# Optimization experiments

Hardware: AMD Instinct MI355X
Metric: run time of the kernel (lower is better)

Reference implementation:

```python
import jax, jax.numpy as jnp
import numpy as np

A, T, N_GRID, RBF, F = 128, 2048, 65536, 16, 128
L_DIMS = (1, 3, 5)  # irreps 0e, 1e, 2e


def setup_inputs() -> dict:
    key = jax.random.key(0)
    ks = jax.random.split(key, 16)
    nrm = lambda k, s, sc=1.0: jax.random.normal(k, s, dtype=jnp.float32) * sc
    w_sc = 1.0 / np.sqrt(F).astype(np.float32)
    return {
        "feat0": nrm(ks[0], (A, F, 1)),
        "feat1": nrm(ks[1], (A, F, 3)),
        "feat2": nrm(ks[2], (A, F, 5)),
        "sph0": nrm(ks[3], (A, T, 1)),
        "sph1": nrm(ks[4], (A, T, 3)),
        "sph2": nrm(ks[5], (A, T, 5)),
        "radial_basis_vals": jax.random.uniform(ks[6], (A, T, RBF), dtype=jnp.float32),
        "mlp_w1": nrm(ks[7], (3, F, F), w_sc),
        "mlp_b1": jnp.zeros((3, F), jnp.float32),
        "mlp_w2": nrm(ks[8], (3, F, F), w_sc),
        "mlp_b2": jnp.zeros((3, F), jnp.float32),
        "mlp_w3": nrm(ks[9], (3, F, RBF * F), w_sc),
        "mlp_b3": jnp.zeros((3, RBF * F), jnp.float32),
        "truncated_idx": jax.random.randint(ks[10], (T,), 0, N_GRID, dtype=jnp.int32),
        "N": N_GRID,
    }


def reference(feat0, feat1, feat2, sph0, sph1, sph2, radial_basis_vals,
              mlp_w1, mlp_b1, mlp_w2, mlp_b2, mlp_w3, mlp_b3,
              truncated_idx, N):
    f_dim = feat0.shape[1]
    rbf = radial_basis_vals.shape[-1]
    inv_features = feat0[..., 0]  # (A, F) scalar (0e) channel
    inv_rbf = jnp.asarray(1.0 / np.sqrt(rbf), dtype=feat0.dtype)
    feats = (feat0, feat1, feat2)
    sphs = (sph0, sph1, sph2)
    spatial_features = jnp.zeros((N, f_dim), dtype=feat0.dtype)
    for i in range(3):  # fixed small loop over irrep chunks
        h = jax.nn.silu(inv_features @ mlp_w1[i] + mlp_b1[i])
        h = jax.nn.silu(h @ mlp_w2[i] + mlp_b2[i])
        rbf_to_f = (h @ mlp_w3[i] + mlp_b3[i]).reshape(-1, rbf, f_dim) * inv_rbf  # (A, RBF, F)
        # reduce over atoms n, sph index d, radial index r -> (T, F)
        sparse = jnp.einsum('ntd,nfd,ntr,nrf->tf', sphs[i], feats[i],
                            radial_basis_vals, rbf_to_f)
        spatial_features = spatial_features.at[truncated_idx].add(sparse)
    return spatial_features
```

## Files before the change

### kernel.cpp

```cpp
#include <hip/hip_runtime.h>
#include <hip/hip_bf16.h>
#include <cstdint>
#include <cstddef>

#define A_DIM 128
#define T_DIM 2048
#define F_DIM 128
#define RBF_DIM 16
#define KDD 2048
#define VT_LD 18432
#define NKG 32
#define BT 64

typedef __attribute__((ext_vector_type(8))) short short8;
typedef __attribute__((ext_vector_type(4))) float f32x4;
typedef __attribute__((ext_vector_type(4))) unsigned int u32x4;

__device__ __forceinline__ float silu_f(float x) {
    return x / (1.0f + __expf(-x));
}

__device__ __forceinline__ unsigned short f2bf(float x) {
    union { float f; unsigned u; } v; v.f = x;
    unsigned r = v.u + 0x7FFFu + ((v.u >> 16) & 1u);
    return (unsigned short)(r >> 16);
}

__device__ __forceinline__ void gl_lds16(const void* g, void* l) {
    __builtin_amdgcn_global_load_lds(
        (const __attribute__((address_space(1))) void*)g,
        (__attribute__((address_space(3))) void*)l, 16, 0, 0);
}

__global__ void zero_kernel(float4* __restrict__ p, int n4) {
    const int stride = gridDim.x * blockDim.x;
    const float4 z = {0.f, 0.f, 0.f, 0.f};
    for (int i = blockIdx.x * blockDim.x + threadIdx.x; i < n4; i += stride)
        p[i] = z;
}

__global__ void mlp_fused_kernel(const float* __restrict__ feat0,
                                 const float* __restrict__ w1, const float* __restrict__ b1,
                                 const float* __restrict__ w2, const float* __restrict__ b2,
                                 const float* __restrict__ w3, const float* __restrict__ b3,
                                 float* __restrict__ rbfws) {
    __shared__ float inv_s[4 * F_DIM];
    __shared__ float h_s[4 * F_DIM];
    __shared__ float h2_s[4 * F_DIM];
    const int i  = blockIdx.y;
    const int a0 = blockIdx.x * 4;
    const int tid = threadIdx.x;
    const int f  = tid & 127;
    const int la = tid >> 7;

    inv_s[tid] = feat0[(a0 + la) * F_DIM + f];
    __syncthreads();

    const float* w1i = w1 + (size_t)i * F_DIM * F_DIM;
    float x = b1[i * F_DIM + f];
    #pragma unroll 8
    for (int k = 0; k < F_DIM; ++k)
        x = fmaf(inv_s[la * F_DIM + k], w1i[k * F_DIM + f], x);
    h_s[tid] = silu_f(x);
    __syncthreads();

    const float* w2i = w2 + (size_t)i * F_DIM * F_DIM;
    float y = b2[i * F_DIM + f];
    #pragma unroll 8
    for (int k = 0; k < F_DIM; ++k)
        y = fmaf(h_s[la * F_DIM + k], w2i[k * F_DIM + f], y);
    h2_s[tid] = silu_f(y);
    __syncthreads();

    const int c = tid * 4;
    const float* w3i = w3 + (size_t)i * F_DIM * 2048;
    float val[4][4];
    #pragma unroll
    for (int a = 0; a < 4; ++a) {
        #pragma unroll
        for (int cc = 0; cc < 4; ++cc)
            val[a][cc] = b3[i * 2048 + c + cc];
    }
    for (int k = 0; k < F_DIM; ++k) {
        const float4 w = *reinterpret_cast<const float4*>(&w3i[(size_t)k * 2048 + c]);
        #pragma unroll
        for (int a = 0; a < 4; ++a) {
            const float h = h2_s[a * F_DIM + k];
            val[a][0] = fmaf(h, w.x, val[a][0]);
            val[a][1] = fmaf(h, w.y, val[a][1]);
            val[a][2] = fmaf(h, w.z, val[a][2]);
            val[a][3] = fmaf(h, w.w, val[a][3]);
        }
    }
    const float inv_rbf = 0.25f;
    #pragma unroll
    for (int a = 0; a < 4; ++a) {
        float4 o;
        o.x = val[a][0] * inv_rbf;
        o.y = val[a][1] * inv_rbf;
        o.z = val[a][2] * inv_rbf;
        o.w = val[a][3] * inv_rbf;
        *reinterpret_cast<float4*>(&rbfws[((size_t)i * A_DIM + a0 + a) * 2048 + c]) = o;
    }
}

__global__ void build_vt_kernel(const float* __restrict__ feat0,
                                const float* __restrict__ feat1,
                                const float* __restrict__ feat2,
                                const float* __restrict__ rbfws,
                                unsigned short* __restrict__ Vt) {
    const int n  = blockIdx.x;
    const int dd = blockIdx.y;
    const int f  = threadIdx.x;

    int i, d;
    float fv;
    if (dd == 0)      { i = 0; d = 0;      fv = feat0[n * F_DIM + f]; }
    else if (dd < 4)  { i = 1; d = dd - 1; fv = feat1[(n * F_DIM + f) * 3 + d]; }
    else              { i = 2; d = dd - 4; fv = feat2[(n * F_DIM + f) * 5 + d]; }

    const float* rb = rbfws + ((size_t)(i * A_DIM + n) * RBF_DIM) * F_DIM + f;
    unsigned short* vp = Vt + (size_t)f * VT_LD + (size_t)dd * KDD + n * 16;
    #pragma unroll
    for (int r = 0; r < RBF_DIM; ++r)
        vp[r] = f2bf(fv * rb[(size_t)r * F_DIM]);
}

template<int MODE>
__global__ void __launch_bounds__(256) gemm_kernel(
        const float* __restrict__ sph0, const float* __restrict__ sph1,
        const float* __restrict__ sph2, const float* __restrict__ radial,
        const unsigned short* __restrict__ Vt,
        float* __restrict__ outbuf,
        float* __restrict__ dout, int out_n4) {
    __shared__ unsigned short b_s[F_DIM * 64];
    __shared__ float sph_s[4 * BT];

    const int tid  = threadIdx.x;
    const int lane = tid & 63;
    const int w    = tid >> 6;
    const int wr   = w >> 1;
    const int wc   = w & 1;
    const int t0   = blockIdx.x * BT + wr * 32;
    const int n0   = blockIdx.y * 4;
    const int kq   = lane >> 4;
    const int lf   = lane & 15;

    if (MODE == 0) {
        const int bid = blockIdx.y * gridDim.x + blockIdx.x;
        const float4 z = {0.f, 0.f, 0.f, 0.f};
        float4* zp = (float4*)dout;
        #pragma unroll
        for (int q = 0; q < 8; ++q) {
            const int idx = bid * 2048 + q * 256 + tid;
            if (idx < out_n4) zp[idx] = z;
        }
    }

    f32x4 rad[2][2][2];
    #pragma unroll
    for (int m = 0; m < 2; ++m) {
        const int t = t0 + 16 * m + lf;
        #pragma unroll
        for (int ks = 0; ks < 2; ++ks) {
            const int n = n0 + 2 * ks + (kq >> 1);
            const float* rp = radial + ((size_t)n * T_DIM + t) * 16 + (kq & 1) * 8;
            rad[m][ks][0] = *reinterpret_cast<const f32x4*>(rp);
            rad[m][ks][1] = *reinterpret_cast<const f32x4*>(rp + 4);
        }
    }

    const int fs_row = tid >> 3;
    const int cs     = (tid & 7) ^ ((tid >> 3) & 7);
    const unsigned short* gsrc0 = Vt + (size_t)fs_row * VT_LD + n0 * 16 + cs * 8;
    const int nn_s = tid >> 6;
    const int tt_s = tid & 63;
    const size_t sph_tbase = (size_t)(n0 + nn_s) * T_DIM + blockIdx.x * BT + tt_s;

    f32x4 acc[2][4];
    #pragma unroll
    for (int m = 0; m < 2; ++m)
        #pragma unroll
        for (int nf = 0; nf < 4; ++nf)
            acc[m][nf] = (f32x4){0.f, 0.f, 0.f, 0.f};

    #pragma unroll 1
    for (int dd = 0; dd < 9; ++dd) {
        const float* sp; int smul, soff;
        if (dd == 0)     { sp = sph0; smul = 1; soff = 0; }
        else if (dd < 4) { sp = sph1; smul = 3; soff = dd - 1; }
        else             { sp = sph2; smul = 5; soff = dd - 4; }

        __syncthreads();

        const size_t koff = (size_t)dd * KDD;
        #pragma unroll
        for (int q = 0; q < 4; ++q) {
            const unsigned short* gp = gsrc0 + koff + (size_t)(q * 32) * VT_LD;
            void* lp = (void*)((char*)b_s + q * 4096 + w * 1024);
            gl_lds16(gp, lp);
        }
        sph_s[tid] = sp[sph_tbase * smul + soff];

        __syncthreads();

        short8 bfr[2][4];
        #pragma unroll
        for (int ks = 0; ks < 2; ++ks) {
            #pragma unroll
            for (int nf = 0; nf < 4; ++nf) {
                const int f = wc * 64 + 16 * nf + lf;
                const int byte = f * 128 + (((ks * 4 + kq) ^ (lf & 7)) * 16);
                bfr[ks][nf] = *reinterpret_cast<const short8*>((const char*)b_s + byte);
            }
        }

        #pragma unroll
        for (int m = 0; m < 2; ++m) {
            #pragma unroll
            for (int ks = 0; ks < 2; ++ks) {
                const float s = sph_s[(2 * ks + (kq >> 1)) * BT + wr * 32 + 16 * m + lf];
                unsigned int d0, d1, d2, d3;
                asm("v_cvt_pk_bf16_f32 %0, %1, %2" : "=v"(d0)
                    : "v"(s * rad[m][ks][0][0]), "v"(s * rad[m][ks][0][1]));
                asm("v_cvt_pk_bf16_f32 %0, %1, %2" : "=v"(d1)
                    : "v"(s * rad[m][ks][0][2]), "v"(s * rad[m][ks][0][3]));
                asm("v_cvt_pk_bf16_f32 %0, %1, %2" : "=v"(d2)
                    : "v"(s * rad[m][ks][1][0]), "v"(s * rad[m][ks][1][1]));
                asm("v_cvt_pk_bf16_f32 %0, %1, %2" : "=v"(d3)
                    : "v"(s * rad[m][ks][1][2]), "v"(s * rad[m][ks][1][3]));
                union { u32x4 u; short8 s8; } au;
                au.u = (u32x4){d0, d1, d2, d3};
                #pragma unroll
                for (int nf = 0; nf < 4; ++nf)
                    acc[m][nf] = __builtin_amdgcn_mfma_f32_16x16x32_bf16(
                        au.s8, bfr[ks][nf], acc[m][nf], 0, 0, 0);
            }
        }
    }

    float* pb = (MODE == 0)
        ? outbuf + (size_t)blockIdx.y * (T_DIM * F_DIM)
        : outbuf;
    #pragma unroll
    for (int m = 0; m < 2; ++m) {
        #pragma unroll
        for (int nf = 0; nf < 4; ++nf) {
            const int f = wc * 64 + 16 * nf + lf;
            #pragma unroll
            for (int reg = 0; reg < 4; ++reg) {
                const int t = t0 + 16 * m + 4 * kq + reg;
                if (MODE == 0)
                    pb[(size_t)t * F_DIM + f] = acc[m][nf][reg];
                else
                    atomicAdd(&pb[(size_t)t * F_DIM + f], acc[m][nf][reg]);
            }
        }
    }
}

__global__ void scatter_sum_kernel(const float* __restrict__ partial,
                                   const int* __restrict__ tidx,
                                   float* __restrict__ out) {
    const int tid = threadIdx.x;
    const int t = blockIdx.x * 2 + (tid >> 7);
    const int f = tid & 127;
    const int g = tidx[t];
    const float* p = partial + (size_t)t * F_DIM + f;
    float s = 0.0f;
    #pragma unroll
    for (int kg = 0; kg < NKG; ++kg)
        s += p[(size_t)kg * (T_DIM * F_DIM)];
    atomicAdd(&out[(size_t)g * F_DIM + f], s);
}

__global__ void scatter_kernel(const float* __restrict__ sparse,
                               const int* __restrict__ tidx,
                               float* __restrict__ out) {
    const int tid = threadIdx.x;
    const int t = blockIdx.x * 2 + (tid >> 7);
    const int f = tid & 127;
    const int g = tidx[t];
    atomicAdd(&out[(size_t)g * F_DIM + f], sparse[(size_t)t * F_DIM + f]);
}

extern "C" void kernel_launch(void* const* d_in, const int* in_sizes, int n_in,
                              void* d_out, int out_size, void* d_ws, size_t ws_size,
                              hipStream_t stream) {
    const float* feat0  = (const float*)d_in[0];
    const float* feat1  = (const float*)d_in[1];
    const float* feat2  = (const float*)d_in[2];
    const float* sph0   = (const float*)d_in[3];
    const float* sph1   = (const float*)d_in[4];
    const float* sph2   = (const float*)d_in[5];
    const float* radial = (const float*)d_in[6];
    const float* w1     = (const float*)d_in[7];
    const float* b1     = (const float*)d_in[8];
    const float* w2     = (const float*)d_in[9];
    const float* b2     = (const float*)d_in[10];
    const float* w3     = (const float*)d_in[11];
    const float* b3     = (const float*)d_in[12];
    const int*   tidx   = (const int*)d_in[13];
    float* out = (float*)d_out;

    float* rbfws  = (float*)d_ws;
    float* h2ws   = rbfws + 3 * A_DIM * RBF_DIM * F_DIM;

    const size_t plain_need =
        (size_t)(3 * A_DIM * RBF_DIM * F_DIM + 3 * A_DIM * F_DIM) * sizeof(float) +
        (size_t)F_DIM * VT_LD * sizeof(unsigned short) +
        (size_t)NKG * T_DIM * F_DIM * sizeof(float);
    const bool plain = (ws_size >= plain_need);

    mlp_fused_kernel<<<dim3(A_DIM / 4, 3), 512, 0, stream>>>(
        feat0, w1, b1, w2, b2, w3, b3, rbfws);

    if (plain) {
        unsigned short* Vt = (unsigned short*)(h2ws + 3 * A_DIM * F_DIM);
        float* partial = (float*)(Vt + (size_t)F_DIM * VT_LD);
        build_vt_kernel<<<dim3(A_DIM, 9), 128, 0, stream>>>(feat0, feat1, feat2, rbfws, Vt);
        gemm_kernel<0><<<dim3(T_DIM / BT, A_DIM / 4), 256, 0, stream>>>(
            sph0, sph1, sph2, radial, Vt, partial, out, out_size / 4);
        scatter_sum_kernel<<<dim3(T_DIM / 2), 256, 0, stream>>>(partial, tidx, out);
    } else {
        float* sparse = h2ws + 3 * A_DIM * F_DIM;
        unsigned short* Vt = (unsigned short*)(sparse + T_DIM * F_DIM);
        zero_kernel<<<2048, 256, 0, stream>>>((float4*)out, out_size / 4);
        hipMemsetAsync(sparse, 0, (size_t)T_DIM * F_DIM * sizeof(float), stream);
        build_vt_kernel<<<dim3(A_DIM, 9), 128, 0, stream>>>(feat0, feat1, feat2, rbfws, Vt);
        gemm_kernel<1><<<dim3(T_DIM / BT, A_DIM / 4), 256, 0, stream>>>(
            sph0, sph1, sph2, radial, Vt, sparse, out, out_size / 4);
        scatter_kernel<<<dim3(T_DIM / 2), 256, 0, stream>>>(sparse, tidx, out);
    }
}
```

Measured before the change: 63.73 us.

## Split fused MLP into two kernels to parallelize final layer and reuse w3

The fused MLP kernel is split into a first/second-layer kernel that writes hidden activations to workspace and a separate third-layer kernel. The third-layer kernel tiles 16 atoms by 128 output columns across a 3D grid of 384 blocks, so each w3 element loaded feeds 8 atoms instead of 4. The old kernel re-read all of w3 from each of 96 blocks. The change costs an extra kernel launch and a global round trip for h2.

```diff
diff --git a/kernel.cpp b/kernel.cpp
--- a/kernel.cpp
+++ b/kernel.cpp
@@ -39,14 +39,12 @@
         p[i] = z;
 }
 
-__global__ void mlp_fused_kernel(const float* __restrict__ feat0,
-                                 const float* __restrict__ w1, const float* __restrict__ b1,
-                                 const float* __restrict__ w2, const float* __restrict__ b2,
-                                 const float* __restrict__ w3, const float* __restrict__ b3,
-                                 float* __restrict__ rbfws) {
+__global__ void mlp12_kernel(const float* __restrict__ feat0,
+                             const float* __restrict__ w1, const float* __restrict__ b1,
+                             const float* __restrict__ w2, const float* __restrict__ b2,
+                             float* __restrict__ h2ws) {
     __shared__ float inv_s[4 * F_DIM];
     __shared__ float h_s[4 * F_DIM];
-    __shared__ float h2_s[4 * F_DIM];
     const int i  = blockIdx.y;
     const int a0 = blockIdx.x * 4;
     const int tid = threadIdx.x;
@@ -69,39 +67,44 @@
     #pragma unroll 8
     for (int k = 0; k < F_DIM; ++k)
         y = fmaf(h_s[la * F_DIM + k], w2i[k * F_DIM + f], y);
-    h2_s[tid] = silu_f(y);
+    h2ws[((size_t)i * A_DIM + a0 + la) * F_DIM + f] = silu_f(y);
+}
+
+__global__ void mlp3_kernel(const float* __restrict__ h2ws,
+                            const float* __restrict__ w3, const float* __restrict__ b3,
+                            float* __restrict__ rbfws) {
+    __shared__ float h2_s[16 * F_DIM];
+    const int i  = blockIdx.z;
+    const int a0 = blockIdx.x * 16;
+    const int c0 = blockIdx.y * 128;
+    const int tid = threadIdx.x;
+
+    #pragma unroll
+    for (int j = 0; j < 8; ++j)
+        h2_s[j * 256 + tid] = h2ws[((size_t)i * A_DIM + a0) * F_DIM + j * 256 + tid];
     __syncthreads();
 
-    const int c = tid * 4;
+    const int la = tid >> 7;
+    const int c  = c0 + (tid & 127);
     const float* w3i = w3 + (size_t)i * F_DIM * 2048;
-    float val[4][4];
-    #pragma unroll
-    for (int a = 0; a < 4; ++a) {
-        #pragma unroll
-        for (int cc = 0; cc < 4; ++cc)
-            val[a][cc] = b3[i * 2048 + c + cc];
-    }
+
+    float val[8];
+    const float b = b3[i * 2048 + c];
+    #pragma unroll
+    for (int a = 0; a < 8; ++a) val[a] = b;
+
+    #pragma unroll 4
     for (int k = 0; k < F_DIM; ++k) {
-        const float4 w = *reinterpret_cast<const float4*>(&w3i[(size_t)k * 2048 + c]);
-        #pragma unroll
-        for (int a = 0; a < 4; ++a) {
-            const float h = h2_s[a * F_DIM + k];
-            val[a][0] = fmaf(h, w.x, val[a][0]);
-            val[a][1] = fmaf(h, w.y, val[a][1]);
-            val[a][2] = fmaf(h, w.z, val[a][2]);
-            val[a][3] = fmaf(h, w.w, val[a][3]);
-        }
-    }
+        const float wv = w3i[(size_t)k * 2048 + c];
+        #pragma unroll
+        for (int a = 0; a < 8; ++a)
+            val[a] = fmaf(h2_s[(la * 8 + a) * F_DIM + k], wv, val[a]);
+    }
+
     const float inv_rbf = 0.25f;
     #pragma unroll
-    for (int a = 0; a < 4; ++a) {
-        float4 o;
-        o.x = val[a][0] * inv_rbf;
-        o.y = val[a][1] * inv_rbf;
-        o.z = val[a][2] * inv_rbf;
-        o.w = val[a][3] * inv_rbf;
-        *reinterpret_cast<float4*>(&rbfws[((size_t)i * A_DIM + a0 + a) * 2048 + c]) = o;
-    }
+    for (int a = 0; a < 8; ++a)
+        rbfws[((size_t)i * A_DIM + a0 + la * 8 + a) * 2048 + c] = val[a] * inv_rbf;
 }
 
 __global__ void build_vt_kernel(const float* __restrict__ feat0,
@@ -312,8 +315,8 @@
         (size_t)NKG * T_DIM * F_DIM * sizeof(float);
     const bool plain = (ws_size >= plain_need);
 
-    mlp_fused_kernel<<<dim3(A_DIM / 4, 3), 512, 0, stream>>>(
-        feat0, w1, b1, w2, b2, w3, b3, rbfws);
+    mlp12_kernel<<<dim3(A_DIM / 4, 3), 512, 0, stream>>>(feat0, w1, b1, w2, b2, h2ws);
+    mlp3_kernel<<<dim3(A_DIM / 16, 16, 3), 256, 0, stream>>>(h2ws, w3, b3, rbfws);
 
     if (plain) {
         unsigned short* Vt = (unsigned short*)(h2ws + 3 * A_DIM * F_DIM);
```

After: 65.27 us. 2.4% more time.
